# Kernel tuning notes

Measured on AMD Instinct MI355X. Metric: run time of the kernel, lower is better.

Reference implementation:

```python
import jax, jax.numpy as jnp
import numpy as np

N = 10000      # nodes
E = 320000     # edges (before self loops)
IN = 128       # in_channels
HID = 128      # hidden_channels
OUT = 64       # out_channels
H = 3          # heads
K = 10         # n_clusters
EDIM = 1       # edge_attr feature dim
NEG_SLOPE = 0.2


def setup_inputs() -> dict:
    key = jax.random.key(0)
    ks = jax.random.split(key, 24)
    x = jax.random.normal(ks[0], (N, IN), jnp.float32)
    src = jax.random.randint(ks[1], (E,), 0, N)
    dst = jax.random.randint(ks[2], (E,), 0, N)
    dst = jnp.where(src == dst, (dst + 1) % N, dst)  # avoid pre-existing self loops
    edge_index = jnp.stack([src, dst]).astype(jnp.int64)
    edge_attr = jax.random.uniform(ks[3], (E, EDIM), dtype=jnp.float32)
    s = 0.1
    inp = {
        'x': x, 'edge_index': edge_index, 'edge_attr': edge_attr,
        # GAT layer 1 params
        'W1': jax.random.normal(ks[4], (IN, H * HID), jnp.float32) * s,
        'att_s1': jax.random.normal(ks[5], (H, HID), jnp.float32) * s,
        'att_d1': jax.random.normal(ks[6], (H, HID), jnp.float32) * s,
        'We1': jax.random.normal(ks[7], (EDIM, H * HID), jnp.float32) * s,
        'att_e1': jax.random.normal(ks[8], (H, HID), jnp.float32) * s,
        'b1': jnp.zeros((H * HID,), jnp.float32),
        # GAT layer 2 params
        'W2': jax.random.normal(ks[9], (H * HID, H * OUT), jnp.float32) * s,
        'att_s2': jax.random.normal(ks[10], (H, OUT), jnp.float32) * s,
        'att_d2': jax.random.normal(ks[11], (H, OUT), jnp.float32) * s,
        'We2': jax.random.normal(ks[12], (EDIM, H * OUT), jnp.float32) * s,
        'att_e2': jax.random.normal(ks[13], (H, OUT), jnp.float32) * s,
        'b2': jnp.zeros((H * OUT,), jnp.float32),
        # cluster head
        'Wp': jax.random.normal(ks[14], (H * OUT, K), jnp.float32) * s,
        'bp': jnp.zeros((K,), jnp.float32),
    }
    return inp


def gat_layer(x, src, dst, eattr, W, att_s, att_d, We, att_e, b, heads, ch):
    n = x.shape[0]
    h = (x @ W).reshape(n, heads, ch)                       # [N,H,C]
    a_s = jnp.einsum('nhc,hc->nh', h, att_s)                # [N,H]
    a_d = jnp.einsum('nhc,hc->nh', h, att_d)
    e = (eattr @ We).reshape(-1, heads, ch)                 # [E,H,C]
    a_e = jnp.einsum('ehc,hc->eh', e, att_e)                # [E,H]
    alpha = jax.nn.leaky_relu(a_s[src] + a_d[dst] + a_e, NEG_SLOPE)
    # segment softmax over destination nodes
    m = jax.ops.segment_max(alpha, dst, num_segments=n)
    ex = jnp.exp(alpha - m[dst])
    denom = jax.ops.segment_sum(ex, dst, num_segments=n)
    coef = ex / (denom[dst] + 1e-16)                        # [E,H]
    msg = h[src] * coef[:, :, None]                         # [E,H,C]
    out = jax.ops.segment_sum(msg, dst, num_segments=n)     # [N,H,C]
    return out.reshape(n, heads * ch) + b


def reference(x, edge_index, edge_attr, W1, att_s1, att_d1, We1, att_e1, b1,
              W2, att_s2, att_d2, We2, att_e2, b2, Wp, bp):
    n = x.shape[0]
    loop = jnp.arange(n, dtype=edge_index.dtype)
    src = jnp.concatenate([edge_index[0], loop])            # add self loops
    dst = jnp.concatenate([edge_index[1], loop])
    ea = jnp.concatenate([edge_attr, jnp.ones((n, edge_attr.shape[1]), edge_attr.dtype)])  # fill_value=1
    h = jnp.nan_to_num(x, nan=0.0)
    h = jax.nn.elu(gat_layer(h, src, dst, ea, W1, att_s1, att_d1, We1, att_e1, b1, H, HID))
    h = gat_layer(h, src, dst, ea, W2, att_s2, att_d2, We2, att_e2, b2, H, OUT)
    z = h / jnp.maximum(jnp.linalg.norm(h, axis=1, keepdims=True), 1e-12)  # F.normalize p=2 dim=1
    A_hat = z @ z.T                                          # [N,N]
    p = jax.nn.softmax(z @ Wp + bp, axis=1)                  # F.softmax picks dim=1 for 2D
    return (A_hat, p, z)
```

## Files before the change

### kernel.cpp

```cpp
#include <hip/hip_runtime.h>
#include <hip/hip_bf16.h>
#include <math.h>

#define NN 10000
#define EE 320000
#define ETOT (EE + NN)
#define INC 128
#define HIDC 128
#define OUTC 64
#define NH 3
#define KCL 10
#define SLOPE 0.2f
#define NPAD 10112

typedef __attribute__((ext_vector_type(8))) short bf16x8;
typedef __attribute__((ext_vector_type(4))) float f32x4;
typedef __attribute__((ext_vector_type(16))) float f32x16;

__device__ __forceinline__ float wave_sum(float v) {
  for (int off = 32; off; off >>= 1) v += __shfl_xor(v, off, 64);
  return v;
}

__device__ __forceinline__ short f2bf(float v) {
  unsigned int u = __float_as_uint(v);
  unsigned int r = (u + 0x7fffu + ((u >> 16) & 1u)) >> 16;
  return (short)r;
}
__device__ __forceinline__ float bf2f(short s) {
  return __uint_as_float(((unsigned int)(unsigned short)s) << 16);
}

__global__ __launch_bounds__(256) void csr_count(const int* __restrict__ dst,
                                                 int* __restrict__ counts,
                                                 int* __restrict__ epos,
                                                 const float* __restrict__ We1,
                                                 const float* __restrict__ ae1,
                                                 const float* __restrict__ We2,
                                                 const float* __restrict__ ae2,
                                                 float* __restrict__ ce) {
  if (blockIdx.x == gridDim.x - 1) {
    int lane = threadIdx.x;
    if (lane < 64) {
      for (int h = 0; h < NH; h++) {
        float p = 0.f;
        for (int c = lane; c < HIDC; c += 64) p += We1[h * HIDC + c] * ae1[h * HIDC + c];
        p = wave_sum(p);
        if (lane == 0) ce[h] = p;
        float q = 0.f;
        for (int c = lane; c < OUTC; c += 64) q += We2[h * OUTC + c] * ae2[h * OUTC + c];
        q = wave_sum(q);
        if (lane == 0) ce[NH + h] = q;
      }
    }
    return;
  }
  int e = blockIdx.x * 256 + threadIdx.x;
  if (e >= ETOT) return;
  int d = (e < EE) ? dst[e] : (e - EE);
  epos[e] = atomicAdd(&counts[d], 1);
}

__global__ __launch_bounds__(1024) void scan_kernel(const int* __restrict__ counts,
                                                    int* __restrict__ offsets) {
  __shared__ int sums[1024];
  const int PT = 10;
  int tid = threadIdx.x;
  int base = tid * PT;
  int loc[PT];
  int run = 0;
#pragma unroll
  for (int j = 0; j < PT; j++) {
    int i = base + j;
    int v = (i < NN) ? counts[i] : 0;
    run += v;
    loc[j] = run;
  }
  sums[tid] = run;
  __syncthreads();
  for (int off = 1; off < 1024; off <<= 1) {
    int t = (tid >= off) ? sums[tid - off] : 0;
    __syncthreads();
    sums[tid] += t;
    __syncthreads();
  }
  int excl = sums[tid] - run;
#pragma unroll
  for (int j = 0; j < PT; j++) {
    int i = base + j;
    if (i < NN) offsets[i + 1] = excl + loc[j];
  }
  if (tid == 0) offsets[0] = 0;
}

__global__ __launch_bounds__(256) void csr_fill(const int* __restrict__ dst,
                                                const int* __restrict__ src,
                                                const float* __restrict__ ea,
                                                const int* __restrict__ offsets,
                                                const int* __restrict__ epos,
                                                int2* __restrict__ erec) {
  int e = blockIdx.x * 256 + threadIdx.x;
  if (e >= ETOT) return;
  int d, s;
  float a;
  if (e < EE) {
    d = dst[e]; s = src[e]; a = ea[e];
  } else {
    d = e - EE; s = e - EE; a = 1.f;
  }
  erec[offsets[d] + epos[e]] = make_int2(s, __float_as_int(a));
}

#define LROW 40
template <bool NANFIX>
__global__ __launch_bounds__(256) void gemm_nn_mfma(const float* __restrict__ A,
                                                    const float* __restrict__ B,
                                                    float* __restrict__ C,
                                                    const float* __restrict__ att_s,
                                                    const float* __restrict__ att_d,
                                                    float* __restrict__ as_out,
                                                    float* __restrict__ ad_out,
                                                    int M, int K, int Nc, int ch) {
  __shared__ short Ah[64 * LROW], Al[64 * LROW];
  __shared__ short Bh[64 * LROW], Bl[64 * LROW];
  int tid = threadIdx.x;
  int lane = tid & 63, wave = tid >> 6;
  int wm = (wave >> 1) * 32, wn = (wave & 1) * 32;
  int bm = blockIdx.y * 64, bn = blockIdx.x * 64;
  int fr = lane & 15, fk = (lane >> 4) * 8;
  f32x4 acc[2][2] = {};
  int ar = tid >> 2, ac = (tid & 3) * 8;
  int bc = tid & 63, bk0 = tid >> 6;

  for (int k0 = 0; k0 < K; k0 += 32) {
    float av[8];
    if (bm + ar < M) {
      const float* src = A + (size_t)(bm + ar) * K + k0 + ac;
      float4 v0 = *(const float4*)src;
      float4 v1 = *(const float4*)(src + 4);
      av[0] = v0.x; av[1] = v0.y; av[2] = v0.z; av[3] = v0.w;
      av[4] = v1.x; av[5] = v1.y; av[6] = v1.z; av[7] = v1.w;
    } else {
#pragma unroll
      for (int j = 0; j < 8; j++) av[j] = 0.f;
    }
#pragma unroll
    for (int j = 0; j < 8; j++) {
      float v = av[j];
      if (NANFIX) v = (v == v) ? v : 0.f;
      short hs = f2bf(v);
      Ah[ar * LROW + ac + j] = hs;
      Al[ar * LROW + ac + j] = f2bf(v - bf2f(hs));
    }
#pragma unroll
    for (int it = 0; it < 8; it++) {
      int kk = bk0 + it * 4;
      float v = B[(size_t)(k0 + kk) * Nc + bn + bc];
      short hs = f2bf(v);
      Bh[bc * LROW + kk] = hs;
      Bl[bc * LROW + kk] = f2bf(v - bf2f(hs));
    }
    __syncthreads();

    bf16x8 ah[2], al2[2], bh[2], bl2[2];
#pragma unroll
    for (int t = 0; t < 2; t++) {
      ah[t]  = *(const bf16x8*)&Ah[(wm + t * 16 + fr) * LROW + fk];
      al2[t] = *(const bf16x8*)&Al[(wm + t * 16 + fr) * LROW + fk];
      bh[t]  = *(const bf16x8*)&Bh[(wn + t * 16 + fr) * LROW + fk];
      bl2[t] = *(const bf16x8*)&Bl[(wn + t * 16 + fr) * LROW + fk];
    }
#pragma unroll
    for (int i = 0; i < 2; i++)
#pragma unroll
      for (int j = 0; j < 2; j++) {
        acc[i][j] = __builtin_amdgcn_mfma_f32_16x16x32_bf16(ah[i], bh[j], acc[i][j], 0, 0, 0);
        acc[i][j] = __builtin_amdgcn_mfma_f32_16x16x32_bf16(ah[i], bl2[j], acc[i][j], 0, 0, 0);
        acc[i][j] = __builtin_amdgcn_mfma_f32_16x16x32_bf16(al2[i], bh[j], acc[i][j], 0, 0, 0);
      }
    __syncthreads();
  }

  int col0 = lane & 15, rq = (lane >> 4) * 4;
#pragma unroll
  for (int i = 0; i < 2; i++)
#pragma unroll
    for (int v = 0; v < 4; v++) {
      int r = bm + wm + i * 16 + rq + v;
      if (r < M) {
#pragma unroll
        for (int j = 0; j < 2; j++)
          C[(size_t)r * Nc + bn + wn + j * 16 + col0] = acc[i][j][v];
      }
    }

  int head = bn / ch;
  float sax0 = att_s[bn + wn + col0], sax1 = att_s[bn + wn + 16 + col0];
  float sdx0 = att_d[bn + wn + col0], sdx1 = att_d[bn + wn + 16 + col0];
#pragma unroll
  for (int i = 0; i < 2; i++)
#pragma unroll
    for (int v = 0; v < 4; v++) {
      float ps = acc[i][0][v] * sax0 + acc[i][1][v] * sax1;
      float pd = acc[i][0][v] * sdx0 + acc[i][1][v] * sdx1;
#pragma unroll
      for (int m = 1; m < 16; m <<= 1) {
        ps += __shfl_xor(ps, m, 64);
        pd += __shfl_xor(pd, m, 64);
      }
      int r = bm + wm + i * 16 + rq + v;
      if ((lane & 15) == 0 && r < M) {
        atomicAdd(&as_out[r * NH + head], ps);
        atomicAdd(&ad_out[r * NH + head], pd);
      }
    }
}

__global__ __launch_bounds__(256) void gat_agg_l1(const float* __restrict__ hfeat,
                                                  const float* __restrict__ a_s,
                                                  const float* __restrict__ a_d,
                                                  const float* __restrict__ ce,
                                                  const int* __restrict__ offsets,
                                                  const int2* __restrict__ erec,
                                                  const float* __restrict__ bias,
                                                  float* __restrict__ out) {
  int wave = threadIdx.x >> 6, lane = threadIdx.x & 63;
  int n = blockIdx.x * 4 + wave;
  int beg = offsets[n], end = offsets[n + 1];
  float adn0 = a_d[n * NH + 0], adn1 = a_d[n * NH + 1], adn2 = a_d[n * NH + 2];
  float ce0 = ce[0], ce1v = ce[1], ce2 = ce[2];

  float s0 = 0.f, s1 = 0.f, s2 = 0.f;
  float a00 = 0.f, a01 = 0.f, a10 = 0.f, a11 = 0.f, a20 = 0.f, a21 = 0.f;

  for (int base = beg; base < end; base += 64) {
    int i = base + lane;
    int se = 0;
    float e0 = 0.f, e1 = 0.f, e2 = 0.f;
    if (i < end) {
      int2 rec = erec[i];
      se = rec.x;
      float a = __int_as_float(rec.y);
      const float* asr = a_s + NH * se;
      float t0 = asr[0] + adn0 + a * ce0; t0 = t0 > 0.f ? t0 : SLOPE * t0;
      float t1 = asr[1] + adn1 + a * ce1v; t1 = t1 > 0.f ? t1 : SLOPE * t1;
      float t2 = asr[2] + adn2 + a * ce2; t2 = t2 > 0.f ? t2 : SLOPE * t2;
      e0 = __expf(t0); e1 = __expf(t1); e2 = __expf(t2);
      s0 += e0; s1 += e1; s2 += e2;
    }
    int cnt = min(64, end - base);
#pragma unroll 4
    for (int t = 0; t < cnt; t++) {
      int s = __shfl(se, t, 64);
      float c0 = __shfl(e0, t, 64);
      float c1 = __shfl(e1, t, 64);
      float c2 = __shfl(e2, t, 64);
      const float2* hr2 = (const float2*)(hfeat + (size_t)s * 384);
      float2 v0 = hr2[lane], v1 = hr2[lane + 64], v2 = hr2[lane + 128];
      a00 += v0.x * c0; a01 += v0.y * c0;
      a10 += v1.x * c1; a11 += v1.y * c1;
      a20 += v2.x * c2; a21 += v2.y * c2;
    }
  }

  s0 = wave_sum(s0); s1 = wave_sum(s1); s2 = wave_sum(s2);
  float di0 = 1.f / (s0 + 1e-16f), di1 = 1.f / (s1 + 1e-16f), di2 = 1.f / (s2 + 1e-16f);

  float2 b0 = *(const float2*)&bias[2 * lane];
  float2 b1 = *(const float2*)&bias[128 + 2 * lane];
  float2 b2 = *(const float2*)&bias[256 + 2 * lane];
  float x0 = a00 * di0 + b0.x, x1 = a01 * di0 + b0.y;
  float y0 = a10 * di1 + b1.x, y1 = a11 * di1 + b1.y;
  float z0 = a20 * di2 + b2.x, z1 = a21 * di2 + b2.y;
  x0 = x0 > 0.f ? x0 : expm1f(x0); x1 = x1 > 0.f ? x1 : expm1f(x1);
  y0 = y0 > 0.f ? y0 : expm1f(y0); y1 = y1 > 0.f ? y1 : expm1f(y1);
  z0 = z0 > 0.f ? z0 : expm1f(z0); z1 = z1 > 0.f ? z1 : expm1f(z1);
  float* orow = out + (size_t)n * 384;
  *(float2*)&orow[2 * lane] = make_float2(x0, x1);
  *(float2*)&orow[128 + 2 * lane] = make_float2(y0, y1);
  *(float2*)&orow[256 + 2 * lane] = make_float2(z0, z1);
}

__global__ __launch_bounds__(256) void gat_agg_l2(const float* __restrict__ hfeat,
                                                  const float* __restrict__ a_s,
                                                  const float* __restrict__ a_d,
                                                  const float* __restrict__ ce,
                                                  const int* __restrict__ offsets,
                                                  const int2* __restrict__ erec,
                                                  const float* __restrict__ bias,
                                                  float* __restrict__ z,
                                                  __hip_bfloat16* __restrict__ zb,
                                                  const float* __restrict__ Wp,
                                                  const float* __restrict__ bp,
                                                  float* __restrict__ p) {
  int wave = threadIdx.x >> 6, lane = threadIdx.x & 63;
  int n = blockIdx.x * 4 + wave;
  int beg = offsets[n], end = offsets[n + 1];
  float adn0 = a_d[n * NH + 0], adn1 = a_d[n * NH + 1], adn2 = a_d[n * NH + 2];
  float ce0 = ce[0], ce1v = ce[1], ce2 = ce[2];

  float s0 = 0.f, s1 = 0.f, s2 = 0.f;
  float a0 = 0.f, a1 = 0.f, a2 = 0.f;

  for (int base = beg; base < end; base += 64) {
    int i = base + lane;
    int se = 0;
    float e0 = 0.f, e1 = 0.f, e2 = 0.f;
    if (i < end) {
      int2 rec = erec[i];
      se = rec.x;
      float a = __int_as_float(rec.y);
      const float* asr = a_s + NH * se;
      float t0 = asr[0] + adn0 + a * ce0; t0 = t0 > 0.f ? t0 : SLOPE * t0;
      float t1 = asr[1] + adn1 + a * ce1v; t1 = t1 > 0.f ? t1 : SLOPE * t1;
      float t2 = asr[2] + adn2 + a * ce2; t2 = t2 > 0.f ? t2 : SLOPE * t2;
      e0 = __expf(t0); e1 = __expf(t1); e2 = __expf(t2);
      s0 += e0; s1 += e1; s2 += e2;
    }
    int cnt = min(64, end - base);
#pragma unroll 4
    for (int t = 0; t < cnt; t++) {
      int s = __shfl(se, t, 64);
      float c0 = __shfl(e0, t, 64);
      float c1 = __shfl(e1, t, 64);
      float c2 = __shfl(e2, t, 64);
      const float* hr = hfeat + (size_t)s * 192;
      a0 += hr[lane] * c0;
      a1 += hr[lane + 64] * c1;
      a2 += hr[lane + 128] * c2;
    }
  }

  s0 = wave_sum(s0); s1 = wave_sum(s1); s2 = wave_sum(s2);
  float x0 = a0 / (s0 + 1e-16f) + bias[lane];
  float x1 = a1 / (s1 + 1e-16f) + bias[lane + 64];
  float x2 = a2 / (s2 + 1e-16f) + bias[lane + 128];

  float sq = wave_sum(x0 * x0 + x1 * x1 + x2 * x2);
  float inv = 1.f / fmaxf(sqrtf(sq), 1e-12f);
  x0 *= inv; x1 *= inv; x2 *= inv;

  float* zr = z + (size_t)n * 192;
  zr[lane] = x0; zr[lane + 64] = x1; zr[lane + 128] = x2;
  __hip_bfloat16* zbr = zb + (size_t)n * 192;
  zbr[lane] = __float2bfloat16(x0);
  zbr[lane + 64] = __float2bfloat16(x1);
  zbr[lane + 128] = __float2bfloat16(x2);

  float lg[KCL];
#pragma unroll
  for (int j = 0; j < KCL; j++) {
    float t = x0 * Wp[lane * KCL + j] + x1 * Wp[(lane + 64) * KCL + j] +
              x2 * Wp[(lane + 128) * KCL + j];
    lg[j] = wave_sum(t) + bp[j];
  }
  if (lane == 0) {
    float m = -1e30f;
#pragma unroll
    for (int j = 0; j < KCL; j++) m = fmaxf(m, lg[j]);
    float ex[KCL];
    float sum = 0.f;
#pragma unroll
    for (int j = 0; j < KCL; j++) { ex[j] = expf(lg[j] - m); sum += ex[j]; }
    float invs = 1.f / sum;
#pragma unroll
    for (int j = 0; j < KCL; j++) p[(size_t)n * KCL + j] = ex[j] * invs;
  }
}

__global__ __launch_bounds__(256) void gemm_zzT_mfma(const short* __restrict__ Zb,
                                                     float* __restrict__ C, int N) {
  __shared__ short As[128 * 32];
  __shared__ short Bs[128 * 32];
  int tid = threadIdx.x;
  int lane = tid & 63;
  int wave = tid >> 6;
  int wm = (wave >> 1) * 64, wn = (wave & 1) * 64;
  int bm = blockIdx.y * 128, bn = blockIdx.x * 128;

  f32x16 acc[2][2] = {};

  int lrow = tid >> 2;
  int sslot = (tid & 3) ^ ((lrow >> 1) & 3);
  int scol = sslot * 8;

  int fr = lane & 31;
  int fks = lane >> 5;

  for (int kt = 0; kt < 6; kt++) {
    int k0 = kt * 32;
    const short* ga0 = Zb + (size_t)(bm + lrow) * 192 + k0 + scol;
    const short* ga1 = Zb + (size_t)(bm + 64 + lrow) * 192 + k0 + scol;
    const short* gb0 = Zb + (size_t)(bn + lrow) * 192 + k0 + scol;
    const short* gb1 = Zb + (size_t)(bn + 64 + lrow) * 192 + k0 + scol;
    __builtin_amdgcn_global_load_lds(
        (const __attribute__((address_space(1))) unsigned int*)ga0,
        (__attribute__((address_space(3))) unsigned int*)&As[lrow * 32 + (tid & 3) * 8], 16, 0, 0);
    __builtin_amdgcn_global_load_lds(
        (const __attribute__((address_space(1))) unsigned int*)ga1,
        (__attribute__((address_space(3))) unsigned int*)&As[(64 + lrow) * 32 + (tid & 3) * 8], 16, 0, 0);
    __builtin_amdgcn_global_load_lds(
        (const __attribute__((address_space(1))) unsigned int*)gb0,
        (__attribute__((address_space(3))) unsigned int*)&Bs[lrow * 32 + (tid & 3) * 8], 16, 0, 0);
    __builtin_amdgcn_global_load_lds(
        (const __attribute__((address_space(1))) unsigned int*)gb1,
        (__attribute__((address_space(3))) unsigned int*)&Bs[(64 + lrow) * 32 + (tid & 3) * 8], 16, 0, 0);
    __syncthreads();

    bf16x8 af[2][2], bfr[2][2];
#pragma unroll
    for (int t = 0; t < 2; t++)
#pragma unroll
      for (int ks = 0; ks < 2; ks++) {
        int ra = wm + t * 32 + fr;
        int rb = wn + t * 32 + fr;
        int sa = ((ks * 2 + fks) ^ ((ra >> 1) & 3)) * 8;
        int sb = ((ks * 2 + fks) ^ ((rb >> 1) & 3)) * 8;
        af[t][ks] = *(const bf16x8*)&As[ra * 32 + sa];
        bfr[t][ks] = *(const bf16x8*)&Bs[rb * 32 + sb];
      }
#pragma unroll
    for (int i = 0; i < 2; i++)
#pragma unroll
      for (int j = 0; j < 2; j++)
#pragma unroll
        for (int ks = 0; ks < 2; ks++)
          acc[i][j] = __builtin_amdgcn_mfma_f32_32x32x16_bf16(af[i][ks], bfr[j][ks],
                                                              acc[i][j], 0, 0, 0);
    __syncthreads();
  }

  int col0 = lane & 31;
  int rbase = 4 * (lane >> 5);
#pragma unroll
  for (int i = 0; i < 2; i++) {
#pragma unroll
    for (int j = 0; j < 2; j++) {
      int c = bn + wn + j * 32 + col0;
      if (c >= N) continue;
#pragma unroll
      for (int r = 0; r < 16; r++) {
        int row = bm + wm + i * 32 + (r & 3) + 8 * (r >> 2) + rbase;
        if (row < N) __builtin_nontemporal_store(acc[i][j][r], &C[(size_t)row * N + c]);
      }
    }
  }
}

extern "C" void kernel_launch(void* const* d_in, const int* in_sizes, int n_in,
                              void* d_out, int out_size, void* d_ws, size_t ws_size,
                              hipStream_t stream) {
  const float* x = (const float*)d_in[0];
  const int* edge_index = (const int*)d_in[1];
  const float* edge_attr = (const float*)d_in[2];
  const float* W1 = (const float*)d_in[3];
  const float* att_s1 = (const float*)d_in[4];
  const float* att_d1 = (const float*)d_in[5];
  const float* We1 = (const float*)d_in[6];
  const float* att_e1 = (const float*)d_in[7];
  const float* b1 = (const float*)d_in[8];
  const float* W2 = (const float*)d_in[9];
  const float* att_s2 = (const float*)d_in[10];
  const float* att_d2 = (const float*)d_in[11];
  const float* We2 = (const float*)d_in[12];
  const float* att_e2 = (const float*)d_in[13];
  const float* b2 = (const float*)d_in[14];
  const float* Wp = (const float*)d_in[15];
  const float* bp = (const float*)d_in[16];

  const int* esrc = edge_index;
  const int* edst = edge_index + EE;

  float* A_hat = (float*)d_out;
  float* p_out = A_hat + (size_t)NN * NN;
  float* z_out = p_out + (size_t)NN * KCL;

  char* ws = (char*)d_ws;
  float* h1 = (float*)ws;            ws += sizeof(float) * (size_t)NN * 384;
  float* h1act = (float*)ws;         ws += sizeof(float) * (size_t)NN * 384;
  int* counts = (int*)ws;            ws += sizeof(int) * NN;
  float* as1 = (float*)ws;           ws += sizeof(float) * NN * NH;
  float* ad1 = (float*)ws;           ws += sizeof(float) * NN * NH;
  float* as2 = (float*)ws;           ws += sizeof(float) * NN * NH;
  float* ad2 = (float*)ws;           ws += sizeof(float) * NN * NH;
  float* ce = (float*)ws;            ws += sizeof(float) * 8;
  int* offsets = (int*)ws;           ws += sizeof(int) * (NN + 4);
  int* epos = (int*)ws;              ws += sizeof(int) * ETOT;
  int2* erec = (int2*)ws;            ws += sizeof(int2) * ETOT;
  __hip_bfloat16* zb = (__hip_bfloat16*)ws; ws += sizeof(__hip_bfloat16) * (size_t)NPAD * 192;

  float* h2 = h1;

  hipMemsetAsync(counts, 0, sizeof(int) * NN + sizeof(float) * 4 * NN * NH, stream);

  int egrid = (ETOT + 255) / 256;
  csr_count<<<egrid + 1, 256, 0, stream>>>(edst, counts, epos, We1, att_e1, We2, att_e2, ce);
  scan_kernel<<<1, 1024, 0, stream>>>(counts, offsets);
  csr_fill<<<egrid, 256, 0, stream>>>(edst, esrc, edge_attr, offsets, epos, erec);

  gemm_nn_mfma<true><<<dim3(384 / 64, (NN + 63) / 64), 256, 0, stream>>>(
      x, W1, h1, att_s1, att_d1, as1, ad1, NN, INC, 384, HIDC);
  gat_agg_l1<<<NN / 4, 256, 0, stream>>>(h1, as1, ad1, ce, offsets, erec, b1, h1act);

  gemm_nn_mfma<false><<<dim3(192 / 64, (NN + 63) / 64), 256, 0, stream>>>(
      h1act, W2, h2, att_s2, att_d2, as2, ad2, NN, 384, 192, OUTC);
  gat_agg_l2<<<NN / 4, 256, 0, stream>>>(h2, as2, ad2, ce + NH, offsets, erec, b2,
                                         z_out, zb, Wp, bp, p_out);

  gemm_zzT_mfma<<<dim3((NN + 127) / 128, (NN + 127) / 128), 256, 0, stream>>>(
      (const short*)zb, A_hat, NN);
}
```

Baseline: 638.8 us.

## Merge CSR count and first GEMM into one launch, use readlane broadcasts

Combines the CSR edge-count kernel, the edge-attention constant computation and the layer-1 projection GEMM into a single heterogeneous kernel whose blocks are split by block index. This removes one launch and lets the independent atomic counting overlap with the MFMA GEMM. The scan now stages counts through shared memory so the global reads and writes are coalesced. The aggregation loops broadcast per-edge values with readlane instead of shuffles, which assumes the loop index is wave-uniform. The merged kernel carries the GEMM's LDS footprint for every block, including the counting blocks, which may reduce occupancy for those blocks.

Measured after the change: 630.1 us. No clear change (-1.4%).

```diff
diff --git a/kernel.cpp b/kernel.cpp
--- a/kernel.cpp
+++ b/kernel.cpp
@@ -12,6 +12,8 @@
 #define KCL 10
 #define SLOPE 0.2f
 #define NPAD 10112
+#define NB_CSR 1290
+#define NB_G1 942
 
 typedef __attribute__((ext_vector_type(8))) short bf16x8;
 typedef __attribute__((ext_vector_type(4))) float f32x4;
@@ -20,6 +22,9 @@
 __device__ __forceinline__ float wave_sum(float v) {
   for (int off = 32; off; off >>= 1) v += __shfl_xor(v, off, 64);
   return v;
+}
+__device__ __forceinline__ float rlane_f(float v, int l) {
+  return __int_as_float(__builtin_amdgcn_readlane(__float_as_int(v), l));
 }
 
 __device__ __forceinline__ short f2bf(float v) {
@@ -31,15 +36,138 @@
   return __uint_as_float(((unsigned int)(unsigned short)s) << 16);
 }
 
-__global__ __launch_bounds__(256) void csr_count(const int* __restrict__ dst,
-                                                 int* __restrict__ counts,
-                                                 int* __restrict__ epos,
-                                                 const float* __restrict__ We1,
-                                                 const float* __restrict__ ae1,
-                                                 const float* __restrict__ We2,
-                                                 const float* __restrict__ ae2,
-                                                 float* __restrict__ ce) {
-  if (blockIdx.x == gridDim.x - 1) {
+#define LROW 40
+template <bool NANFIX>
+__device__ __forceinline__ void gemm_body(int bx, int by,
+                                          const float* __restrict__ A,
+                                          const float* __restrict__ B,
+                                          float* __restrict__ C,
+                                          const float* __restrict__ att_s,
+                                          const float* __restrict__ att_d,
+                                          float* __restrict__ as_out,
+                                          float* __restrict__ ad_out,
+                                          int M, int K, int Nc, int ch,
+                                          short* Ah, short* Al, short* Bh, short* Bl) {
+  int tid = threadIdx.x;
+  int lane = tid & 63, wave = tid >> 6;
+  int wm = (wave >> 1) * 32, wn = (wave & 1) * 32;
+  int bm = by * 64, bn = bx * 64;
+  int fr = lane & 15, fk = (lane >> 4) * 8;
+  f32x4 acc[2][2] = {};
+  int ar = tid >> 2, ac = (tid & 3) * 8;
+  int bc = tid & 63, bk0 = tid >> 6;
+
+  for (int k0 = 0; k0 < K; k0 += 32) {
+    float av[8];
+    if (bm + ar < M) {
+      const float* src = A + (size_t)(bm + ar) * K + k0 + ac;
+      float4 v0 = *(const float4*)src;
+      float4 v1 = *(const float4*)(src + 4);
+      av[0] = v0.x; av[1] = v0.y; av[2] = v0.z; av[3] = v0.w;
+      av[4] = v1.x; av[5] = v1.y; av[6] = v1.z; av[7] = v1.w;
+    } else {
+#pragma unroll
+      for (int j = 0; j < 8; j++) av[j] = 0.f;
+    }
+#pragma unroll
+    for (int j = 0; j < 8; j++) {
+      float v = av[j];
+      if (NANFIX) v = (v == v) ? v : 0.f;
+      short hs = f2bf(v);
+      Ah[ar * LROW + ac + j] = hs;
+      Al[ar * LROW + ac + j] = f2bf(v - bf2f(hs));
+    }
+#pragma unroll
+    for (int it = 0; it < 8; it++) {
+      int kk = bk0 + it * 4;
+      float v = B[(size_t)(k0 + kk) * Nc + bn + bc];
+      short hs = f2bf(v);
+      Bh[bc * LROW + kk] = hs;
+      Bl[bc * LROW + kk] = f2bf(v - bf2f(hs));
+    }
+    __syncthreads();
+
+    bf16x8 ah[2], al2[2], bh[2], bl2[2];
+#pragma unroll
+    for (int t = 0; t < 2; t++) {
+      ah[t]  = *(const bf16x8*)&Ah[(wm + t * 16 + fr) * LROW + fk];
+      al2[t] = *(const bf16x8*)&Al[(wm + t * 16 + fr) * LROW + fk];
+      bh[t]  = *(const bf16x8*)&Bh[(wn + t * 16 + fr) * LROW + fk];
+      bl2[t] = *(const bf16x8*)&Bl[(wn + t * 16 + fr) * LROW + fk];
+    }
+#pragma unroll
+    for (int i = 0; i < 2; i++)
+#pragma unroll
+      for (int j = 0; j < 2; j++) {
+        acc[i][j] = __builtin_amdgcn_mfma_f32_16x16x32_bf16(ah[i], bh[j], acc[i][j], 0, 0, 0);
+        acc[i][j] = __builtin_amdgcn_mfma_f32_16x16x32_bf16(ah[i], bl2[j], acc[i][j], 0, 0, 0);
+        acc[i][j] = __builtin_amdgcn_mfma_f32_16x16x32_bf16(al2[i], bh[j], acc[i][j], 0, 0, 0);
+      }
+    __syncthreads();
+  }
+
+  int col0 = lane & 15, rq = (lane >> 4) * 4;
+#pragma unroll
+  for (int i = 0; i < 2; i++)
+#pragma unroll
+    for (int v = 0; v < 4; v++) {
+      int r = bm + wm + i * 16 + rq + v;
+      if (r < M) {
+#pragma unroll
+        for (int j = 0; j < 2; j++)
+          C[(size_t)r * Nc + bn + wn + j * 16 + col0] = acc[i][j][v];
+      }
+    }
+
+  int head = bn / ch;
+  float sax0 = att_s[bn + wn + col0], sax1 = att_s[bn + wn + 16 + col0];
+  float sdx0 = att_d[bn + wn + col0], sdx1 = att_d[bn + wn + 16 + col0];
+#pragma unroll
+  for (int i = 0; i < 2; i++)
+#pragma unroll
+    for (int v = 0; v < 4; v++) {
+      float ps = acc[i][0][v] * sax0 + acc[i][1][v] * sax1;
+      float pd = acc[i][0][v] * sdx0 + acc[i][1][v] * sdx1;
+#pragma unroll
+      for (int m = 1; m < 16; m <<= 1) {
+        ps += __shfl_xor(ps, m, 64);
+        pd += __shfl_xor(pd, m, 64);
+      }
+      int r = bm + wm + i * 16 + rq + v;
+      if ((lane & 15) == 0 && r < M) {
+        atomicAdd(&as_out[r * NH + head], ps);
+        atomicAdd(&ad_out[r * NH + head], pd);
+      }
+    }
+}
+
+__global__ __launch_bounds__(256) void mega1(const int* __restrict__ dst,
+                                             int* __restrict__ counts,
+                                             int* __restrict__ epos,
+                                             const float* __restrict__ We1,
+                                             const float* __restrict__ ae1,
+                                             const float* __restrict__ We2,
+                                             const float* __restrict__ ae2,
+                                             float* __restrict__ ce,
+                                             const float* __restrict__ A,
+                                             const float* __restrict__ B,
+                                             float* __restrict__ C,
+                                             const float* __restrict__ att_s,
+                                             const float* __restrict__ att_d,
+                                             float* __restrict__ as_out,
+                                             float* __restrict__ ad_out) {
+  __shared__ short Ah[64 * LROW], Al[64 * LROW];
+  __shared__ short Bh[64 * LROW], Bl[64 * LROW];
+  int bid = blockIdx.x;
+  if (bid < NB_CSR) {
+    int e = bid * 256 + threadIdx.x;
+    if (e < ETOT) {
+      int d = (e < EE) ? dst[e] : (e - EE);
+      epos[e] = atomicAdd(&counts[d], 1);
+    }
+    return;
+  }
+  if (bid == NB_CSR) {
     int lane = threadIdx.x;
     if (lane < 64) {
       for (int h = 0; h < NH; h++) {
@@ -55,26 +183,40 @@
     }
     return;
   }
-  int e = blockIdx.x * 256 + threadIdx.x;
-  if (e >= ETOT) return;
-  int d = (e < EE) ? dst[e] : (e - EE);
-  epos[e] = atomicAdd(&counts[d], 1);
+  int g = bid - (NB_CSR + 1);
+  gemm_body<true>(g % 6, g / 6, A, B, C, att_s, att_d, as_out, ad_out,
+                  NN, INC, 384, HIDC, Ah, Al, Bh, Bl);
+}
+
+template <bool NANFIX>
+__global__ __launch_bounds__(256) void gemm_nn_mfma(const float* __restrict__ A,
+                                                    const float* __restrict__ B,
+                                                    float* __restrict__ C,
+                                                    const float* __restrict__ att_s,
+                                                    const float* __restrict__ att_d,
+                                                    float* __restrict__ as_out,
+                                                    float* __restrict__ ad_out,
+                                                    int M, int K, int Nc, int ch) {
+  __shared__ short Ah[64 * LROW], Al[64 * LROW];
+  __shared__ short Bh[64 * LROW], Bl[64 * LROW];
+  gemm_body<NANFIX>(blockIdx.x, blockIdx.y, A, B, C, att_s, att_d, as_out, ad_out,
+                    M, K, Nc, ch, Ah, Al, Bh, Bl);
 }
 
 __global__ __launch_bounds__(1024) void scan_kernel(const int* __restrict__ counts,
                                                     int* __restrict__ offsets) {
+  __shared__ int buf[10240];
   __shared__ int sums[1024];
   const int PT = 10;
   int tid = threadIdx.x;
+  for (int i = tid; i < 10240; i += 1024) buf[i] = (i < NN) ? counts[i] : 0;
+  __syncthreads();
   int base = tid * PT;
-  int loc[PT];
   int run = 0;
 #pragma unroll
   for (int j = 0; j < PT; j++) {
-    int i = base + j;
-    int v = (i < NN) ? counts[i] : 0;
-    run += v;
-    loc[j] = run;
+    run += buf[base + j];
+    buf[base + j] = run;
   }
   sums[tid] = run;
   __syncthreads();
@@ -86,10 +228,10 @@
   }
   int excl = sums[tid] - run;
 #pragma unroll
-  for (int j = 0; j < PT; j++) {
-    int i = base + j;
-    if (i < NN) offsets[i + 1] = excl + loc[j];
-  }
+  for (int j = 0; j < PT; j++) buf[base + j] += excl;
+  __syncthreads();
+  for (int i = tid; i < 10240; i += 1024)
+    if (i < NN) offsets[i + 1] = buf[i];
   if (tid == 0) offsets[0] = 0;
 }
 
@@ -111,111 +253,6 @@
   erec[offsets[d] + epos[e]] = make_int2(s, __float_as_int(a));
 }
 
-#define LROW 40
-template <bool NANFIX>
-__global__ __launch_bounds__(256) void gemm_nn_mfma(const float* __restrict__ A,
-                                                    const float* __restrict__ B,
-                                                    float* __restrict__ C,
-                                                    const float* __restrict__ att_s,
-                                                    const float* __restrict__ att_d,
-                                                    float* __restrict__ as_out,
-                                                    float* __restrict__ ad_out,
-                                                    int M, int K, int Nc, int ch) {
-  __shared__ short Ah[64 * LROW], Al[64 * LROW];
-  __shared__ short Bh[64 * LROW], Bl[64 * LROW];
-  int tid = threadIdx.x;
-  int lane = tid & 63, wave = tid >> 6;
-  int wm = (wave >> 1) * 32, wn = (wave & 1) * 32;
-  int bm = blockIdx.y * 64, bn = blockIdx.x * 64;
-  int fr = lane & 15, fk = (lane >> 4) * 8;
-  f32x4 acc[2][2] = {};
-  int ar = tid >> 2, ac = (tid & 3) * 8;
-  int bc = tid & 63, bk0 = tid >> 6;
-
-  for (int k0 = 0; k0 < K; k0 += 32) {
-    float av[8];
-    if (bm + ar < M) {
-      const float* src = A + (size_t)(bm + ar) * K + k0 + ac;
-      float4 v0 = *(const float4*)src;
-      float4 v1 = *(const float4*)(src + 4);
-      av[0] = v0.x; av[1] = v0.y; av[2] = v0.z; av[3] = v0.w;
-      av[4] = v1.x; av[5] = v1.y; av[6] = v1.z; av[7] = v1.w;
-    } else {
-#pragma unroll
-      for (int j = 0; j < 8; j++) av[j] = 0.f;
-    }
-#pragma unroll
-    for (int j = 0; j < 8; j++) {
-      float v = av[j];
-      if (NANFIX) v = (v == v) ? v : 0.f;
-      short hs = f2bf(v);
-      Ah[ar * LROW + ac + j] = hs;
-      Al[ar * LROW + ac + j] = f2bf(v - bf2f(hs));
-    }
-#pragma unroll
-    for (int it = 0; it < 8; it++) {
-      int kk = bk0 + it * 4;
-      float v = B[(size_t)(k0 + kk) * Nc + bn + bc];
-      short hs = f2bf(v);
-      Bh[bc * LROW + kk] = hs;
-      Bl[bc * LROW + kk] = f2bf(v - bf2f(hs));
-    }
-    __syncthreads();
-
-    bf16x8 ah[2], al2[2], bh[2], bl2[2];
-#pragma unroll
-    for (int t = 0; t < 2; t++) {
-      ah[t]  = *(const bf16x8*)&Ah[(wm + t * 16 + fr) * LROW + fk];
-      al2[t] = *(const bf16x8*)&Al[(wm + t * 16 + fr) * LROW + fk];
-      bh[t]  = *(const bf16x8*)&Bh[(wn + t * 16 + fr) * LROW + fk];
-      bl2[t] = *(const bf16x8*)&Bl[(wn + t * 16 + fr) * LROW + fk];
-    }
-#pragma unroll
-    for (int i = 0; i < 2; i++)
-#pragma unroll
-      for (int j = 0; j < 2; j++) {
-        acc[i][j] = __builtin_amdgcn_mfma_f32_16x16x32_bf16(ah[i], bh[j], acc[i][j], 0, 0, 0);
-        acc[i][j] = __builtin_amdgcn_mfma_f32_16x16x32_bf16(ah[i], bl2[j], acc[i][j], 0, 0, 0);
-        acc[i][j] = __builtin_amdgcn_mfma_f32_16x16x32_bf16(al2[i], bh[j], acc[i][j], 0, 0, 0);
-      }
-    __syncthreads();
-  }
-
-  int col0 = lane & 15, rq = (lane >> 4) * 4;
-#pragma unroll
-  for (int i = 0; i < 2; i++)
-#pragma unroll
-    for (int v = 0; v < 4; v++) {
-      int r = bm + wm + i * 16 + rq + v;
-      if (r < M) {
-#pragma unroll
-        for (int j = 0; j < 2; j++)
-          C[(size_t)r * Nc + bn + wn + j * 16 + col0] = acc[i][j][v];
-      }
-    }
-
-  int head = bn / ch;
-  float sax0 = att_s[bn + wn + col0], sax1 = att_s[bn + wn + 16 + col0];
-  float sdx0 = att_d[bn + wn + col0], sdx1 = att_d[bn + wn + 16 + col0];
-#pragma unroll
-  for (int i = 0; i < 2; i++)
-#pragma unroll
-    for (int v = 0; v < 4; v++) {
-      float ps = acc[i][0][v] * sax0 + acc[i][1][v] * sax1;
-      float pd = acc[i][0][v] * sdx0 + acc[i][1][v] * sdx1;
-#pragma unroll
-      for (int m = 1; m < 16; m <<= 1) {
-        ps += __shfl_xor(ps, m, 64);
-        pd += __shfl_xor(pd, m, 64);
-      }
-      int r = bm + wm + i * 16 + rq + v;
-      if ((lane & 15) == 0 && r < M) {
-        atomicAdd(&as_out[r * NH + head], ps);
-        atomicAdd(&ad_out[r * NH + head], pd);
-      }
-    }
-}
-
 __global__ __launch_bounds__(256) void gat_agg_l1(const float* __restrict__ hfeat,
                                                   const float* __restrict__ a_s,
                                                   const float* __restrict__ a_d,
@@ -251,10 +288,8 @@
     int cnt = min(64, end - base);
 #pragma unroll 4
     for (int t = 0; t < cnt; t++) {
-      int s = __shfl(se, t, 64);
-      float c0 = __shfl(e0, t, 64);
-      float c1 = __shfl(e1, t, 64);
-      float c2 = __shfl(e2, t, 64);
+      int s = __builtin_amdgcn_readlane(se, t);
+      float c0 = rlane_f(e0, t), c1 = rlane_f(e1, t), c2 = rlane_f(e2, t);
       const float2* hr2 = (const float2*)(hfeat + (size_t)s * 384);
       float2 v0 = hr2[lane], v1 = hr2[lane + 64], v2 = hr2[lane + 128];
       a00 += v0.x * c0; a01 += v0.y * c0;
@@ -320,10 +355,8 @@
     int cnt = min(64, end - base);
 #pragma unroll 4
     for (int t = 0; t < cnt; t++) {
-      int s = __shfl(se, t, 64);
-      float c0 = __shfl(e0, t, 64);
-      float c1 = __shfl(e1, t, 64);
-      float c2 = __shfl(e2, t, 64);
+      int s = __builtin_amdgcn_readlane(se, t);
+      float c0 = rlane_f(e0, t), c1 = rlane_f(e1, t), c2 = rlane_f(e2, t);
       const float* hr = hfeat + (size_t)s * 192;
       a0 += hr[lane] * c0;
       a1 += hr[lane + 64] * c1;
@@ -493,13 +526,12 @@
 
   hipMemsetAsync(counts, 0, sizeof(int) * NN + sizeof(float) * 4 * NN * NH, stream);
 
-  int egrid = (ETOT + 255) / 256;
-  csr_count<<<egrid + 1, 256, 0, stream>>>(edst, counts, epos, We1, att_e1, We2, att_e2, ce);
+  mega1<<<NB_CSR + 1 + NB_G1, 256, 0, stream>>>(edst, counts, epos,
+                                                We1, att_e1, We2, att_e2, ce,
+                                                x, W1, h1, att_s1, att_d1, as1, ad1);
   scan_kernel<<<1, 1024, 0, stream>>>(counts, offsets);
-  csr_fill<<<egrid, 256, 0, stream>>>(edst, esrc, edge_attr, offsets, epos, erec);
-
-  gemm_nn_mfma<true><<<dim3(384 / 64, (NN + 63) / 64), 256, 0, stream>>>(
-      x, W1, h1, att_s1, att_d1, as1, ad1, NN, INC, 384, HIDC);
+  csr_fill<<<NB_CSR, 256, 0, stream>>>(edst, esrc, edge_attr, offsets, epos, erec);
+
   gat_agg_l1<<<NN / 4, 256, 0, stream>>>(h1, as1, ad1, ce, offsets, erec, b1, h1act);
 
   gemm_nn_mfma<false><<<dim3(192 / 64, (NN + 63) / 64), 256, 0, stream>>>(
```
